# Kernel tuning notes

Hardware: AMD Instinct MI355X
Metric: run time of the kernel (lower is better)

## Reference

```python
import jax, jax.numpy as jnp
import numpy as np

FIELD = 7  # field_size


def _conv1x1(x, w):
    # x: [b,c,h,w], w: [c_out,c_in] (1x1 conv, no bias)
    return jnp.einsum('bchw,oc->bohw', x, w)


def _patches(x, f):
    # torch unfold with 'same' padding: output [b, c*f*f, h, w], channel-major
    # (feature index = c*f*f + kh*f + kw), matching KAIR extract_image_patches
    # layout for odd f / stride 1 (symmetric pad (f-1)//2).
    return jax.lax.conv_general_dilated_patches(
        x, filter_shape=(f, f), window_strides=(1, 1), padding='SAME',
        dimension_numbers=('NCHW', 'OIHW', 'NCHW'))


def setup_inputs() -> dict:
    key = jax.random.key(0)
    k0, k1, k2, k3, k4 = jax.random.split(key, 5)
    c, ci = 256, 128
    b, h, w = 4, 64, 64
    s = 1.0 / np.sqrt(c)
    si = 1.0 / np.sqrt(ci)
    return {
        'x': jax.random.normal(k0, (b, c, h, w), dtype=jnp.float32),
        'w_phi': jax.random.normal(k1, (ci, c), dtype=jnp.float32) * s,
        'w_theta': jax.random.normal(k2, (ci, c), dtype=jnp.float32) * s,
        'w_g': jax.random.normal(k3, (ci, c), dtype=jnp.float32) * s,
        'w_mask': jax.random.normal(k4, (c, ci), dtype=jnp.float32) * si,
    }


def reference(x, w_phi, w_theta, w_g, w_mask):
    b, c, h, w = x.shape
    ci = w_phi.shape[0]
    f = FIELD
    kk = f * f

    x_phi = _conv1x1(x, w_phi)      # [b,ci,h,w]
    x_g = _conv1x1(x, w_g)          # [b,ci,h,w]
    x_theta = _conv1x1(x, w_theta)  # [b,ci,h,w]

    # theta: unsqueeze(-2) then permute(0,2,4,3,1) -> [b,h,w,1,ci]
    q = jnp.transpose(x_theta, (0, 2, 3, 1))[:, :, :, None, :]

    # phi patches: [b, ci*kk, h, w] reshaped (row-major, faithful to torch
    # reshape of the unfold output) to [b,h,w,ci,kk]
    p_phi = _patches(x_phi, f).reshape(b, h, w, ci, kk)
    scores = jnp.matmul(q, p_phi)                 # [b,h,w,1,kk]
    attn = jax.nn.softmax(scores, axis=1)         # softmax over dim=1 (h), faithful

    p_g = _patches(x_g, f).reshape(b, h, w, kk, ci)
    out = jnp.matmul(attn, p_g)                   # [b,h,w,1,ci]

    # permute(0,4,3,1,2).view(b,ci,h,w)
    y = jnp.transpose(out, (0, 4, 3, 1, 2)).reshape(b, ci, h, w)
    mask = _conv1x1(y, w_mask)                    # [b,c,h,w]
    return mask + x
```

## Files before the change

### kernel.cpp

```cpp
#include <hip/hip_runtime.h>


#define PLANE    5040
#define A_BATCH  645120

typedef __attribute__((ext_vector_type(8))) short short8;
typedef __attribute__((ext_vector_type(4))) float floatx4;

__device__ __forceinline__ float bf2f(unsigned short u) {
    union { unsigned int i; float f; } v; v.i = ((unsigned int)u) << 16; return v.f;
}
__device__ __forceinline__ unsigned short f2bf(float f) {
    union { float f; unsigned int i; } v; v.f = f;
    unsigned int r = v.i + 0x7FFFu + ((v.i >> 16) & 1u);
    return (unsigned short)(r >> 16);
}

__device__ __forceinline__ unsigned off_of_ch(int ch) {
    int c0 = ch / 49; if (c0 > 127) c0 = 127;
    int rr = ch - c0 * 49;
    int kh = rr / 7;
    int kw = rr - kh * 7;
    return (unsigned)(c0 * PLANE + kh * 72 + kw + 1);
}

__global__ __launch_bounds__(256) void prep_kernel(
    const float* __restrict__ x,
    const float* __restrict__ w_phi,
    const float* __restrict__ w_theta,
    const float* __restrict__ w_g,
    const float* __restrict__ w_mask,
    unsigned short* __restrict__ xp_hi,
    unsigned short* __restrict__ xp_lo,
    unsigned short* __restrict__ w3p_hi,
    unsigned short* __restrict__ w3p_lo,
    unsigned short* __restrict__ wmp_hi,
    unsigned short* __restrict__ wmp_lo,
    uint4* __restrict__ zero_region)
{
    const int tid = threadIdx.x;
    const int bx = blockIdx.x;

    if (bx < 1024) {
        const int b  = bx >> 8;
        const int kt = (bx >> 6) & 3;
        const int pt = bx & 63;
        __shared__ float tile[64][65];
        #pragma unroll
        for (int i = 0; i < 16; ++i) {
            int lin = tid + i * 256;
            int kk = lin >> 6, pp = lin & 63;
            tile[kk][pp] = x[(b * 256 + kt * 64 + kk) * 4096 + pt * 64 + pp];
        }
        __syncthreads();
        #pragma unroll
        for (int i = 0; i < 16; ++i) {
            int lin = tid + i * 256;
            int frag = lin >> 9;
            int idx  = lin & 511;
            int kbL  = frag >> 2;
            int ptL  = frag & 3;
            int j    = idx & 7;
            int n    = (idx >> 3) & 15;
            int quad = idx >> 7;
            float f = tile[kbL * 32 + quad * 8 + j][ptL * 16 + n];
            unsigned short h = f2bf(f);
            int addr = ((b * 8 + kt * 2 + kbL) * 256 + pt * 4 + ptL) * 512 + idx;
            xp_hi[addr] = h;
            xp_lo[addr] = f2bf(f - bf2f(h));
        }
    } else {
        const int wid = (bx - 1024) * 256 + tid;
        for (int e = wid; e < 98304; e += 32768) {
            int frag = e >> 9;
            int idx  = e & 511;
            int nt16 = frag >> 3, kb = frag & 7;
            int j = idx & 7, m = (idx >> 3) & 15, quad = idx >> 7;
            int n = nt16 * 16 + m;
            int k = kb * 32 + quad * 8 + j;
            float v = (n < 128) ? w_phi[n * 256 + k]
                    : (n < 256) ? w_theta[(n - 128) * 256 + k]
                                : w_g[(n - 256) * 256 + k];
            unsigned short h = f2bf(v);
            w3p_hi[e] = h;
            w3p_lo[e] = f2bf(v - bf2f(h));
        }
        {
            int e = wid;
            int frag = e >> 9;
            int idx  = e & 511;
            int ot16 = frag >> 2, kb = frag & 3;
            int j = idx & 7, m = (idx >> 3) & 15, quad = idx >> 7;
            float v = w_mask[(ot16 * 16 + m) * 128 + kb * 32 + quad * 8 + j];
            unsigned short h = f2bf(v);
            wmp_hi[e] = h;
            wmp_lo[e] = f2bf(v - bf2f(h));
        }
        const uint4 z = make_uint4(0u, 0u, 0u, 0u);
        for (int i = wid; i < 645120; i += 32768) zero_region[i] = z;
    }
}

__global__ __launch_bounds__(256) void conv3_mfma_kernel(
    const unsigned short* __restrict__ xp_hi,
    const unsigned short* __restrict__ xp_lo,
    const unsigned short* __restrict__ w3p_hi,
    const unsigned short* __restrict__ w3p_lo,
    unsigned short* __restrict__ A_phi,
    unsigned short* __restrict__ theta_bf,
    unsigned short* __restrict__ A_g)
{
    const int tid = threadIdx.x;
    const int w   = tid >> 6;
    const int ln  = tid & 63;
    const int lm  = ln & 15;
    const int quad = ln >> 4;
    const int bx = blockIdx.x;
    const int nt = blockIdx.y;
    const int b  = blockIdx.z;
    const int nt16a = nt * 8 + w;
    const int nt16b = nt * 8 + 4 + w;
    const int lnofs = ln * 8;

    floatx4 accA[4] = {{0.f,0.f,0.f,0.f},{0.f,0.f,0.f,0.f},
                       {0.f,0.f,0.f,0.f},{0.f,0.f,0.f,0.f}};
    floatx4 accB[4] = {{0.f,0.f,0.f,0.f},{0.f,0.f,0.f,0.f},
                       {0.f,0.f,0.f,0.f},{0.f,0.f,0.f,0.f}};

    #pragma unroll
    for (int kb = 0; kb < 8; ++kb) {
        const int aoffA = (nt16a * 8 + kb) * 512 + lnofs;
        const int aoffB = (nt16b * 8 + kb) * 512 + lnofs;
        const int boff  = ((b * 8 + kb) * 256 + bx * 4) * 512 + lnofs;
        short8 ahA = *reinterpret_cast<const short8*>(w3p_hi + aoffA);
        short8 alA = *reinterpret_cast<const short8*>(w3p_lo + aoffA);
        short8 ahB = *reinterpret_cast<const short8*>(w3p_hi + aoffB);
        short8 alB = *reinterpret_cast<const short8*>(w3p_lo + aoffB);
        short8 bh[4], bl[4];
        #pragma unroll
        for (int ct = 0; ct < 4; ++ct) {
            bh[ct] = *reinterpret_cast<const short8*>(xp_hi + boff + ct * 512);
            bl[ct] = *reinterpret_cast<const short8*>(xp_lo + boff + ct * 512);
        }
        #pragma unroll
        for (int ct = 0; ct < 4; ++ct) {
            accA[ct] = __builtin_amdgcn_mfma_f32_16x16x32_bf16(ahA, bh[ct], accA[ct], 0, 0, 0);
            accA[ct] = __builtin_amdgcn_mfma_f32_16x16x32_bf16(ahA, bl[ct], accA[ct], 0, 0, 0);
            accA[ct] = __builtin_amdgcn_mfma_f32_16x16x32_bf16(alA, bh[ct], accA[ct], 0, 0, 0);
            accB[ct] = __builtin_amdgcn_mfma_f32_16x16x32_bf16(ahB, bh[ct], accB[ct], 0, 0, 0);
            accB[ct] = __builtin_amdgcn_mfma_f32_16x16x32_bf16(ahB, bl[ct], accB[ct], 0, 0, 0);
            accB[ct] = __builtin_amdgcn_mfma_f32_16x16x32_bf16(alB, bh[ct], accB[ct], 0, 0, 0);
        }
    }

    const int py = bx;
    if (nt == 1) {
        #pragma unroll
        for (int ct = 0; ct < 4; ++ct) {
            const int p = bx * 64 + ct * 16 + lm;
            #pragma unroll
            for (int reg = 0; reg < 4; ++reg) {
                const int r = w * 16 + quad * 4 + reg;
                theta_bf[(b * 4096 + p) * 128 + r]      = f2bf(accA[ct][reg]);
                theta_bf[(b * 4096 + p) * 128 + r + 64] = f2bf(accB[ct][reg]);
            }
        }
    } else {
        unsigned short* __restrict__ A = (nt == 0) ? A_phi : A_g;
        #pragma unroll
        for (int ct = 0; ct < 4; ++ct) {
            const int pxx = ct * 16 + lm;
            #pragma unroll
            for (int reg = 0; reg < 4; ++reg) {
                const int r = w * 16 + quad * 4 + reg;
                A[b * A_BATCH + r * PLANE + (py + 3) * 72 + pxx + 4] =
                    f2bf(accA[ct][reg]);
                A[b * A_BATCH + (r + 64) * PLANE + (py + 3) * 72 + pxx + 4] =
                    f2bf(accB[ct][reg]);
            }
        }
    }
}

__global__ __launch_bounds__(1024, 8) void scores_kernel(
    const unsigned short* __restrict__ Apad,
    const unsigned short* __restrict__ theta_bf,
    float* __restrict__ scores)
{
    const int tid = threadIdx.x;
    const int w   = tid >> 6;
    const int ln  = tid & 63;
    const int s0  = blockIdx.x * 16;
    const int b   = blockIdx.y;
    const int s   = s0 + w;

    __shared__ float th[16][128];
    __shared__ unsigned short sA[9600];

    {
        int idx = tid * 2;
        int lp = idx >> 7, cc = idx & 127;
        const unsigned short* tb = theta_bf + (b * 4096 + s0 + lp) * 128 + cc;
        th[lp][cc]     = bf2f(tb[0]);
        th[lp][cc + 1] = bf2f(tb[1]);
    }

    const int chB_lo = (s0 * 6272) >> 12;
    int chB_hi = ((s0 + 15) * 6272 + 6286) >> 12;
    if (chB_hi > 6271) chB_hi = 6271;
    const unsigned a_base = off_of_ch(chB_lo);
    const int cnt = (int)(off_of_ch(chB_hi) + 4599u - a_base) + 1;

    {
        const unsigned short* src = Apad + b * A_BATCH + a_base;
        for (int i = tid; i < cnt; i += 1024) sA[i] = src[i];
    }
    __syncthreads();

    const int base  = s * 6272;
    const int ch_lo = base >> 12;
    const unsigned B1 = (unsigned)(ch_lo + 1) << 12;
    const unsigned B2 = (unsigned)(ch_lo + 2) << 12;
    const int d1 = (int)B1 - base;
    const int d2 = d1 + 4096;

    int A1 = d1 / 49;
    int A2 = (d1 + 48) / 49;
    int C1 = d2 / 49;        if (C1 > 128) C1 = 128;
    int C2 = (d2 + 48) / 49; if (C2 > 128) C2 = 128;

    unsigned OFFv[3];
    #pragma unroll
    for (int i = 0; i < 3; ++i)
        OFFv[i] = off_of_ch(ch_lo + i) - a_base;

    unsigned F = (unsigned)(base + ln);
    float acc = 0.f;

    {
        const unsigned OFF_ = OFFv[0];
        #pragma unroll 4
        for (int cc = 0; cc < A1; ++cc) {
            unsigned p = F & 4095u;
            unsigned a = OFF_ + p + ((p >> 6) << 3);
            acc = fmaf(th[w][cc], bf2f(sA[a]), acc);
            F += 49u;
        }
    }
    for (int cc = A1; cc < A2; ++cc) {
        unsigned OFF_ = (F >= B1) ? OFFv[1] : OFFv[0];
        unsigned p = F & 4095u;
        unsigned a = OFF_ + p + ((p >> 6) << 3);
        acc = fmaf(th[w][cc], bf2f(sA[a]), acc);
        F += 49u;
    }
    {
        const unsigned OFF_ = OFFv[1];
        #pragma unroll 4
        for (int cc = A2; cc < C1; ++cc) {
            unsigned p = F & 4095u;
            unsigned a = OFF_ + p + ((p >> 6) << 3);
            acc = fmaf(th[w][cc], bf2f(sA[a]), acc);
            F += 49u;
        }
    }
    for (int cc = C1; cc < C2; ++cc) {
        unsigned OFF_ = (F >= B2) ? OFFv[2] : OFFv[1];
        unsigned p = F & 4095u;
        unsigned a = OFF_ + p + ((p >> 6) << 3);
        acc = fmaf(th[w][cc], bf2f(sA[a]), acc);
        F += 49u;
    }
    {
        const unsigned OFF_ = OFFv[2];
        #pragma unroll 4
        for (int cc = C2; cc < 128; ++cc) {
            unsigned p = F & 4095u;
            unsigned a = OFF_ + p + ((p >> 6) << 3);
            acc = fmaf(th[w][cc], bf2f(sA[a]), acc);
            F += 49u;
        }
    }

    if (ln < 49) scores[(b * 4096 + s) * 64 + ln] = acc;
}

__global__ __launch_bounds__(256) void softmax_stats_kernel(
    const float* __restrict__ scores,
    float* __restrict__ m_arr,
    float* __restrict__ inv_arr)
{
    const int b = blockIdx.x >> 6;
    const int j = blockIdx.x & 63;
    const int tid = threadIdx.x;
    const int wv = tid >> 6;
    const int ln = tid & 63;

    __shared__ float tile[64][52];

    #pragma unroll
    for (int it = 0; it < 16; ++it) {
        int i = it * 4 + wv;
        if (ln < 49) tile[i][ln] = scores[(b * 4096 + i * 64 + j) * 64 + ln];
    }
    __syncthreads();

    if (tid < 49) {
        float m = -3.4e38f;
        #pragma unroll 8
        for (int i = 0; i < 64; ++i) m = fmaxf(m, tile[i][tid]);
        float sum = 0.f;
        #pragma unroll 8
        for (int i = 0; i < 64; ++i) sum += __expf(tile[i][tid] - m);
        m_arr[(b * 64 + j) * 49 + tid]   = m;
        inv_arr[(b * 64 + j) * 49 + tid] = 1.f / sum;
    }
}

__global__ __launch_bounds__(1024) void agg_mask_kernel(
    const float* __restrict__ scores,
    const float* __restrict__ m_arr,
    const float* __restrict__ inv_arr,
    const unsigned short* __restrict__ Apad,
    const unsigned short* __restrict__ wmp_hi,
    const unsigned short* __restrict__ wmp_lo,
    const float* __restrict__ x,
    float* __restrict__ out)
{
    const int tid = threadIdx.x;
    const int blk = blockIdx.x;
    const int b   = blockIdx.y;
    const int P0  = blk * 32;

    __shared__ float at_l[32][52];
    __shared__ unsigned short y_lds[8 * 512];

    const int j0 = P0 & 63;
    #pragma unroll
    for (int it = 0; it < 2; ++it) {
        int idx = tid + it * 1024;
        int lp = idx >> 6;
        int t  = idx & 63;
        if (t < 49) {
            const int s = P0 + lp;
            const int j = j0 + lp;
            float sc = scores[(b * 4096 + s) * 64 + t];
            float m  = m_arr[(b * 64 + j) * 49 + t];
            float iv = inv_arr[(b * 64 + j) * 49 + t];
            at_l[lp][t] = __expf(sc - m) * iv;
        }
    }
    __syncthreads();

    const unsigned short* __restrict__ Ab = Apad + b * A_BATCH;
    const int pq = tid >> 7;
    const int cc = tid & 127;

    #pragma unroll
    for (int rep = 0; rep < 4; ++rep) {
        const int lp = rep * 8 + pq;
        const int s  = P0 + lp;

        const int base  = s * 6272;
        const int ch_lo = base >> 12;
        const unsigned B1 = (unsigned)(ch_lo + 1) << 12;
        const unsigned B2 = (unsigned)(ch_lo + 2) << 12;
        const int d1 = (int)B1 - base;
        const int d2 = d1 + 4096;

        int A1 = d1 >> 7;
        int A2 = (d1 + 127) >> 7;
        int C1 = d2 >> 7;          if (C1 > 49) C1 = 49;
        int C2 = (d2 + 127) >> 7;  if (C2 > 49) C2 = 49;
        if (A1 > 49) A1 = 49;
        if (A2 > 49) A2 = 49;

        unsigned OFFv[3];
        #pragma unroll
        for (int i = 0; i < 3; ++i) {
            int ch = ch_lo + i;
            int c0 = ch / 49; if (c0 > 127) c0 = 127;
            int rr = ch - c0 * 49;
            int kh = rr / 7;
            int kw = rr - kh * 7;
            OFFv[i] = (unsigned)(c0 * PLANE + kh * 72 + kw + 1);
        }

        float acc = 0.f;

        {
            unsigned p0 = (unsigned)(base + cc) & 4095u;
            unsigned a = OFFv[0] + p0 + ((p0 >> 6) << 3);
            #pragma unroll 4
            for (int t = 0; t < A1; ++t) {
                acc = fmaf(at_l[lp][t], bf2f(Ab[a]), acc);
                a += 144u;
            }
        }
        for (int t = A1; t < A2; ++t) {
            unsigned F = (unsigned)(base + cc) + 128u * (unsigned)t;
            unsigned OFF_ = (F >= B1) ? OFFv[1] : OFFv[0];
            unsigned p = F & 4095u;
            unsigned a = OFF_ + p + ((p >> 6) << 3);
            acc = fmaf(at_l[lp][t], bf2f(Ab[a]), acc);
        }
        {
            unsigned F = (unsigned)(base + cc) + 128u * (unsigned)A2;
            unsigned p0 = F & 4095u;
            unsigned a = OFFv[1] + p0 + ((p0 >> 6) << 3);
            #pragma unroll 4
            for (int t = A2; t < C1; ++t) {
                acc = fmaf(at_l[lp][t], bf2f(Ab[a]), acc);
                a += 144u;
            }
        }
        for (int t = C1; t < C2; ++t) {
            unsigned F = (unsigned)(base + cc) + 128u * (unsigned)t;
            unsigned OFF_ = (F >= B2) ? OFFv[2] : OFFv[1];
            unsigned p = F & 4095u;
            unsigned a = OFF_ + p + ((p >> 6) << 3);
            acc = fmaf(at_l[lp][t], bf2f(Ab[a]), acc);
        }
        {
            unsigned F = (unsigned)(base + cc) + 128u * (unsigned)C2;
            unsigned p0 = F & 4095u;
            unsigned a = OFFv[2] + p0 + ((p0 >> 6) << 3);
            #pragma unroll 4
            for (int t = C2; t < 49; ++t) {
                acc = fmaf(at_l[lp][t], bf2f(Ab[a]), acc);
                a += 144u;
            }
        }

        const int kb = cc >> 5, k32 = cc & 31;
        const int quad = k32 >> 3, jx = k32 & 7;
        const int ct = lp >> 4, n = lp & 15;
        y_lds[(kb * 2 + ct) * 512 + (quad * 16 + n) * 8 + jx] = f2bf(acc);
    }
    __syncthreads();

    const int w    = tid >> 6;
    const int ln   = tid & 63;
    const int lm   = ln & 15;
    const int quad = ln >> 4;
    const int lnofs = ln * 8;

    floatx4 accA[2] = {{0.f,0.f,0.f,0.f},{0.f,0.f,0.f,0.f}};

    #pragma unroll
    for (int kb = 0; kb < 4; ++kb) {
        const int aoffA = (w * 4 + kb) * 512 + lnofs;
        short8 ahA = *reinterpret_cast<const short8*>(wmp_hi + aoffA);
        short8 alA = *reinterpret_cast<const short8*>(wmp_lo + aoffA);
        short8 bf[2];
        #pragma unroll
        for (int ct = 0; ct < 2; ++ct)
            bf[ct] = *reinterpret_cast<const short8*>(
                y_lds + (kb * 2 + ct) * 512 + lnofs);
        #pragma unroll
        for (int ct = 0; ct < 2; ++ct) {
            accA[ct] = __builtin_amdgcn_mfma_f32_16x16x32_bf16(ahA, bf[ct], accA[ct], 0, 0, 0);
            accA[ct] = __builtin_amdgcn_mfma_f32_16x16x32_bf16(alA, bf[ct], accA[ct], 0, 0, 0);
        }
    }

    #pragma unroll
    for (int ct = 0; ct < 2; ++ct) {
        const int p = P0 + ct * 16 + lm;
        #pragma unroll
        for (int reg = 0; reg < 4; ++reg) {
            const int oA = w * 16 + quad * 4 + reg;
            const int ofsA = (b * 256 + oA) * 4096 + p;
            out[ofsA] = accA[ct][reg] + x[ofsA];
        }
    }
}

extern "C" void kernel_launch(void* const* d_in, const int* in_sizes, int n_in,
                              void* d_out, int out_size, void* d_ws, size_t ws_size,
                              hipStream_t stream) {
    const float* x       = (const float*)d_in[0];
    const float* w_phi   = (const float*)d_in[1];
    const float* w_theta = (const float*)d_in[2];
    const float* w_g     = (const float*)d_in[3];
    const float* w_mask  = (const float*)d_in[4];

    float* out_f = (float*)d_out;

    unsigned short* ws_u  = (unsigned short*)d_ws;
    unsigned short* A_phi = ws_u;
    unsigned short* A_g   = ws_u + 2580480;
    unsigned short* th_u  = ws_u + 7258112;
    float*          sc_f  = (float*)(ws_u + 9355264);
    unsigned short* xph   = ws_u + 11452416;
    unsigned short* xpl   = ws_u + 15646720;
    unsigned short* w3ph  = ws_u + 19841024;
    unsigned short* w3pl  = ws_u + 19939328;
    unsigned short* wmph  = ws_u + 20037632;
    unsigned short* wmpl  = ws_u + 20070400;
    float*          m_f   = (float*)(ws_u + 20103168);
    float*          inv_f = (float*)(ws_u + 20128256);

    hipLaunchKernelGGL(prep_kernel, dim3(1152), dim3(256), 0, stream,
                       x, w_phi, w_theta, w_g, w_mask,
                       xph, xpl, w3ph, w3pl, wmph, wmpl, (uint4*)A_phi);
    hipLaunchKernelGGL(conv3_mfma_kernel, dim3(64, 3, 4), dim3(256), 0, stream,
                       xph, xpl, w3ph, w3pl, A_phi, th_u, A_g);
    hipLaunchKernelGGL(scores_kernel, dim3(256, 4), dim3(1024), 0, stream,
                       A_phi, th_u, sc_f);
    hipLaunchKernelGGL(softmax_stats_kernel, dim3(256), dim3(256), 0, stream,
                       sc_f, m_f, inv_f);
    hipLaunchKernelGGL(agg_mask_kernel, dim3(128, 4), dim3(1024), 0, stream,
                       sc_f, m_f, inv_f, A_g, wmph, wmpl, x, out_f);
}
```

Baseline: 159.1 us.

## Stage g-patch window in LDS for aggregation and halve conv tile width

The aggregation kernel now copies the contiguous span of the padded g buffer that its 32 positions touch into shared memory once per block. The inner weighted sums then read from LDS instead of making scattered global loads, and offsets are rebased to the start of that span. Separately, the 1x1 conv MFMA kernel processes 32 pixels per block instead of 64, doubling the grid to raise occupancy. The costs are about 19 KB of extra LDS per block, which may limit residency, and extra B-operand traffic from the smaller conv tiles.

New measurement: 156.2 us. Within noise of the previous version (-1.8%).

```diff
diff --git a/kernel.cpp b/kernel.cpp
--- a/kernel.cpp
+++ b/kernel.cpp
@@ -122,28 +122,26 @@
     const int nt16b = nt * 8 + 4 + w;
     const int lnofs = ln * 8;
 
-    floatx4 accA[4] = {{0.f,0.f,0.f,0.f},{0.f,0.f,0.f,0.f},
-                       {0.f,0.f,0.f,0.f},{0.f,0.f,0.f,0.f}};
-    floatx4 accB[4] = {{0.f,0.f,0.f,0.f},{0.f,0.f,0.f,0.f},
-                       {0.f,0.f,0.f,0.f},{0.f,0.f,0.f,0.f}};
+    floatx4 accA[2] = {{0.f,0.f,0.f,0.f},{0.f,0.f,0.f,0.f}};
+    floatx4 accB[2] = {{0.f,0.f,0.f,0.f},{0.f,0.f,0.f,0.f}};
 
     #pragma unroll
     for (int kb = 0; kb < 8; ++kb) {
         const int aoffA = (nt16a * 8 + kb) * 512 + lnofs;
         const int aoffB = (nt16b * 8 + kb) * 512 + lnofs;
-        const int boff  = ((b * 8 + kb) * 256 + bx * 4) * 512 + lnofs;
+        const int boff  = ((b * 8 + kb) * 256 + bx * 2) * 512 + lnofs;
         short8 ahA = *reinterpret_cast<const short8*>(w3p_hi + aoffA);
         short8 alA = *reinterpret_cast<const short8*>(w3p_lo + aoffA);
         short8 ahB = *reinterpret_cast<const short8*>(w3p_hi + aoffB);
         short8 alB = *reinterpret_cast<const short8*>(w3p_lo + aoffB);
-        short8 bh[4], bl[4];
-        #pragma unroll
-        for (int ct = 0; ct < 4; ++ct) {
+        short8 bh[2], bl[2];
+        #pragma unroll
+        for (int ct = 0; ct < 2; ++ct) {
             bh[ct] = *reinterpret_cast<const short8*>(xp_hi + boff + ct * 512);
             bl[ct] = *reinterpret_cast<const short8*>(xp_lo + boff + ct * 512);
         }
         #pragma unroll
-        for (int ct = 0; ct < 4; ++ct) {
+        for (int ct = 0; ct < 2; ++ct) {
             accA[ct] = __builtin_amdgcn_mfma_f32_16x16x32_bf16(ahA, bh[ct], accA[ct], 0, 0, 0);
             accA[ct] = __builtin_amdgcn_mfma_f32_16x16x32_bf16(ahA, bl[ct], accA[ct], 0, 0, 0);
             accA[ct] = __builtin_amdgcn_mfma_f32_16x16x32_bf16(alA, bh[ct], accA[ct], 0, 0, 0);
@@ -153,11 +151,13 @@
         }
     }
 
-    const int py = bx;
+    const int py   = bx >> 1;
+    const int px32 = (bx & 1) * 32;
+
     if (nt == 1) {
         #pragma unroll
-        for (int ct = 0; ct < 4; ++ct) {
-            const int p = bx * 64 + ct * 16 + lm;
+        for (int ct = 0; ct < 2; ++ct) {
+            const int p = bx * 32 + ct * 16 + lm;
             #pragma unroll
             for (int reg = 0; reg < 4; ++reg) {
                 const int r = w * 16 + quad * 4 + reg;
@@ -168,15 +168,14 @@
     } else {
         unsigned short* __restrict__ A = (nt == 0) ? A_phi : A_g;
         #pragma unroll
-        for (int ct = 0; ct < 4; ++ct) {
-            const int pxx = ct * 16 + lm;
+        for (int ct = 0; ct < 2; ++ct) {
+            const int pxx = px32 + ct * 16 + lm;
+            const int pbase = (py + 3) * 72 + pxx + 4;
             #pragma unroll
             for (int reg = 0; reg < 4; ++reg) {
                 const int r = w * 16 + quad * 4 + reg;
-                A[b * A_BATCH + r * PLANE + (py + 3) * 72 + pxx + 4] =
-                    f2bf(accA[ct][reg]);
-                A[b * A_BATCH + (r + 64) * PLANE + (py + 3) * 72 + pxx + 4] =
-                    f2bf(accB[ct][reg]);
+                A[b * A_BATCH + r * PLANE + pbase]        = f2bf(accA[ct][reg]);
+                A[b * A_BATCH + (r + 64) * PLANE + pbase] = f2bf(accB[ct][reg]);
             }
         }
     }
@@ -334,6 +333,7 @@
 
     __shared__ float at_l[32][52];
     __shared__ unsigned short y_lds[8 * 512];
+    __shared__ unsigned short sA[9728];
 
     const int j0 = P0 & 63;
     #pragma unroll
@@ -350,9 +350,18 @@
             at_l[lp][t] = __expf(sc - m) * iv;
         }
     }
+
+    const int chB_lo = (P0 * 6272) >> 12;
+    int chB_hi = ((P0 + 31) * 6272 + 6271) >> 12;
+    if (chB_hi > 6271) chB_hi = 6271;
+    const unsigned a_base = off_of_ch(chB_lo);
+    const int cnt = (int)(off_of_ch(chB_hi) + 4599u - a_base) + 1;
+    {
+        const unsigned short* src = Apad + b * A_BATCH + a_base;
+        for (int i = tid; i < cnt; i += 1024) sA[i] = src[i];
+    }
     __syncthreads();
 
-    const unsigned short* __restrict__ Ab = Apad + b * A_BATCH;
     const int pq = tid >> 7;
     const int cc = tid & 127;
 
@@ -377,14 +386,8 @@
 
         unsigned OFFv[3];
         #pragma unroll
-        for (int i = 0; i < 3; ++i) {
-            int ch = ch_lo + i;
-            int c0 = ch / 49; if (c0 > 127) c0 = 127;
-            int rr = ch - c0 * 49;
-            int kh = rr / 7;
-            int kw = rr - kh * 7;
-            OFFv[i] = (unsigned)(c0 * PLANE + kh * 72 + kw + 1);
-        }
+        for (int i = 0; i < 3; ++i)
+            OFFv[i] = off_of_ch(ch_lo + i) - a_base;
 
         float acc = 0.f;
 
@@ -393,7 +396,7 @@
             unsigned a = OFFv[0] + p0 + ((p0 >> 6) << 3);
             #pragma unroll 4
             for (int t = 0; t < A1; ++t) {
-                acc = fmaf(at_l[lp][t], bf2f(Ab[a]), acc);
+                acc = fmaf(at_l[lp][t], bf2f(sA[a]), acc);
                 a += 144u;
             }
         }
@@ -402,7 +405,7 @@
             unsigned OFF_ = (F >= B1) ? OFFv[1] : OFFv[0];
             unsigned p = F & 4095u;
             unsigned a = OFF_ + p + ((p >> 6) << 3);
-            acc = fmaf(at_l[lp][t], bf2f(Ab[a]), acc);
+            acc = fmaf(at_l[lp][t], bf2f(sA[a]), acc);
         }
         {
             unsigned F = (unsigned)(base + cc) + 128u * (unsigned)A2;
@@ -410,7 +413,7 @@
             unsigned a = OFFv[1] + p0 + ((p0 >> 6) << 3);
             #pragma unroll 4
             for (int t = A2; t < C1; ++t) {
-                acc = fmaf(at_l[lp][t], bf2f(Ab[a]), acc);
+                acc = fmaf(at_l[lp][t], bf2f(sA[a]), acc);
                 a += 144u;
             }
         }
@@ -419,7 +422,7 @@
             unsigned OFF_ = (F >= B2) ? OFFv[2] : OFFv[1];
             unsigned p = F & 4095u;
             unsigned a = OFF_ + p + ((p >> 6) << 3);
-            acc = fmaf(at_l[lp][t], bf2f(Ab[a]), acc);
+            acc = fmaf(at_l[lp][t], bf2f(sA[a]), acc);
         }
         {
             unsigned F = (unsigned)(base + cc) + 128u * (unsigned)C2;
@@ -427,7 +430,7 @@
             unsigned a = OFFv[2] + p0 + ((p0 >> 6) << 3);
             #pragma unroll 4
             for (int t = C2; t < 49; ++t) {
-                acc = fmaf(at_l[lp][t], bf2f(Ab[a]), acc);
+                acc = fmaf(at_l[lp][t], bf2f(sA[a]), acc);
                 a += 144u;
             }
         }
@@ -504,7 +507,7 @@
     hipLaunchKernelGGL(prep_kernel, dim3(1152), dim3(256), 0, stream,
                        x, w_phi, w_theta, w_g, w_mask,
                        xph, xpl, w3ph, w3pl, wmph, wmpl, (uint4*)A_phi);
-    hipLaunchKernelGGL(conv3_mfma_kernel, dim3(64, 3, 4), dim3(256), 0, stream,
+    hipLaunchKernelGGL(conv3_mfma_kernel, dim3(128, 3, 4), dim3(256), 0, stream,
                        xph, xpl, w3ph, w3pl, A_phi, th_u, A_g);
     hipLaunchKernelGGL(scores_kernel, dim3(256, 4), dim3(1024), 0, stream,
                        A_phi, th_u, sc_f);
```
